# Kernel tuning notes

Hardware: AMD Instinct MI355X
Metric: run time of the kernel (lower is better)

Reference implementation:

```python
import jax, jax.numpy as jnp
import numpy as np

SAMPLE_RATE = 256
WIN = 64          # round(256*250/1000)
HOP = 32          # round(256*125/1000)
HIDDEN = 512
PER_CHAN = 8
MAX_CH = 64
_EEG_BANDS = ((0.5, 4.0), (4.0, 8.0), (8.0, 13.0), (13.0, 30.0), (30.0, 100.0))

_FREQS = np.fft.rfftfreq(WIN, d=1.0 / SAMPLE_RATE)
_BAND_MASKS = [np.logical_and(_FREQS >= lo, _FREQS < hi) for (lo, hi) in _EEG_BANDS]


def _sinusoidal_1d(n, dim, dtype=jnp.float32):
    pos = jnp.arange(n, dtype=jnp.float32)[:, None]
    half = dim // 2
    div = jnp.exp(jnp.arange(half, dtype=jnp.float32) * (-np.log(10000.0) / half))
    ang = pos * div[None, :]
    pe = jnp.zeros((n, dim), dtype=jnp.float32)
    pe = pe.at[:, 0::2].set(jnp.sin(ang))
    pe = pe.at[:, 1::2].set(jnp.cos(ang))
    return pe.astype(dtype)


def setup_inputs() -> dict:
    key = jax.random.key(0)
    k = jax.random.split(key, 5)
    B, T, C = 8, 65536, 64
    return {
        "signal": jax.random.normal(k[0], (B, T, C), dtype=jnp.float32),
        "chan_w": 0.02 * jax.random.normal(k[1], (MAX_CH, 7, PER_CHAN), dtype=jnp.float32),
        "chan_b": 0.02 * jax.random.normal(k[2], (MAX_CH, PER_CHAN), dtype=jnp.float32),
        "mix_w": 0.02 * jax.random.normal(k[3], (HIDDEN, MAX_CH * PER_CHAN), dtype=jnp.float32),
        "marker": 0.02 * jax.random.normal(k[4], (HIDDEN,), dtype=jnp.float32),
    }


def reference(signal, chan_w, chan_b, mix_w, marker):
    B, T, C = signal.shape  # C == MAX_CH, no padding/mask branch
    Tw = (T - WIN) // HOP + 1
    idx = jnp.arange(Tw)[:, None] * HOP + jnp.arange(WIN)[None, :]
    x = jnp.transpose(signal[:, idx, :], (0, 1, 3, 2))
    # spectral features
    mag = jnp.abs(jnp.fft.rfft(x, axis=-1))
    band_feats = jnp.stack(
        [mag[..., m].mean(axis=-1) if m.any() else jnp.zeros(mag.shape[:-1], mag.dtype)
         for m in _BAND_MASKS],
        axis=-1,
    )  # (B, Tw, C, 5)
    mean = x.mean(axis=-1, keepdims=True)
    std = jnp.std(x, axis=-1, ddof=1, keepdims=True)  # torch std is unbiased
    feats = jnp.concatenate([band_feats, mean, std], axis=-1)  # (B, Tw, C, 7)
    # per-channel projection + bias
    emb = jnp.einsum("btcf,cfp->btcp", feats, chan_w) + chan_b[None, None]
    flat = emb.reshape(B, Tw, MAX_CH * PER_CHAN)
    z = flat @ mix_w.T  # (B, Tw, HIDDEN)
    z = z + _sinusoidal_1d(Tw, HIDDEN, z.dtype)[None]
    mk = jnp.broadcast_to(marker[None, None, :], (B, 1, HIDDEN))
    return jnp.concatenate([mk, z], axis=1)  # (B, 1+Tw, HIDDEN)
```

## Files before the change

### kernel.cpp

```cpp
#include <hip/hip_runtime.h>
#include <hip/hip_bf16.h>
#include <stdint.h>

#define TW_N 2047
#define BATCH 8
#define T_LEN 65536
#define NCH 64
#define HID 512
#define NWIN (BATCH * TW_N)

typedef unsigned short ushortT;

__device__ __forceinline__ ushortT f2b(float f) {
  union { float f; uint32_t i; } v; v.f = f;
  uint32_t r = v.i + 0x7fffu + ((v.i >> 16) & 1u);
  return (ushortT)(r >> 16);
}
__device__ __forceinline__ uint32_t pk2(float lo, float hi) {
  return (uint32_t)f2b(lo) | ((uint32_t)f2b(hi) << 16);
}

constexpr float CQ[17] = {
  1.0f, 0.9951847267f, 0.9807852804f, 0.9569403357f, 0.9238795325f,
  0.8819212643f, 0.8314696123f, 0.7730104534f, 0.7071067812f, 0.6343932842f,
  0.5555702330f, 0.4713967368f, 0.3826834324f, 0.2902846773f, 0.1950903220f,
  0.0980171403f, 0.0f };
constexpr float cos64(int m) {
  m &= 63;
  return (m <= 16) ? CQ[m] : (m < 32) ? -CQ[32 - m] : (m < 48) ? -CQ[m - 32] : CQ[64 - m];
}
constexpr float sin64(int m) { return cos64(m - 16); }
struct TwTab { float c[24][32]; float s[24][32]; };
constexpr TwTab make_tab() {
  TwTab t{};
  for (int i = 0; i < 24; ++i)
    for (int j = 0; j < 32; ++j) {
      int m = ((i + 1) * j) & 63;
      t.c[i][j] = cos64(m);
      t.s[i][j] = sin64(m);
    }
  return t;
}
constexpr TwTab TT = make_tab();

__global__ __launch_bounds__(256) void marker_kernel(
    const float* __restrict__ marker, float* __restrict__ out)
{
  const int idx = blockIdx.x * 256 + threadIdx.x;
  out[(size_t)(idx >> 9) * (2048 * 512) + (idx & 511)] = marker[idx & 511];
}

__global__ __launch_bounds__(256) void feat_embed_kernel(
    const float* __restrict__ sig, const float* __restrict__ chw,
    const float* __restrict__ chb, ushortT* __restrict__ flatB)
{
  const int wv = threadIdx.x >> 6;
  const int c = threadIdx.x & 63;
  const int w = blockIdx.x * 4 + wv;
  const int b = w / TW_N;
  const int tw = w - b * TW_N;
  const size_t base = ((size_t)(b * T_LEN + tw * 32)) * NCH + c;

  float x[64];
#pragma unroll
  for (int t = 0; t < 64; ++t) x[t] = sig[base + (size_t)t * NCH];

  float sum = 0.f, sumsq = 0.f;
#pragma unroll
  for (int t = 0; t < 64; ++t) { sum += x[t]; sumsq = fmaf(x[t], x[t], sumsq); }

  float e[32], o[32];
#pragma unroll
  for (int t = 0; t < 32; ++t) { e[t] = x[t] + x[t + 32]; o[t] = x[t] - x[t + 32]; }

  float b1 = 0.f, b2 = 0.f, b3 = 0.f, b4 = 0.f;
#pragma unroll
  for (int i = 0; i < 24; ++i) {
    const int k = i + 1;
    float re = 0.f, im = 0.f;
#pragma unroll
    for (int t = 0; t < 32; ++t) {
      const float v = (k & 1) ? o[t] : e[t];
      re = fmaf(v, TT.c[i][t], re);
      im = fmaf(v, TT.s[i][t], im);
    }
    const float mag = sqrtf(fmaf(re, re, im * im));
    if (k == 1) b1 += mag;
    else if (k < 4) b2 += mag;
    else if (k < 8) b3 += mag;
    else b4 += mag;
  }

  const float mean = sum * (1.f / 64.f);
  const float var = (sumsq - sum * sum * (1.f / 64.f)) * (1.f / 63.f);
  const float sd = sqrtf(fmaxf(var, 0.f));

  float feats[7];
  feats[0] = 0.f;
  feats[1] = b1;
  feats[2] = b2 * 0.5f;
  feats[3] = b3 * 0.25f;
  feats[4] = b4 * (1.f / 17.f);
  feats[5] = mean;
  feats[6] = sd;

  const float* wr = chw + c * 56;
  float emb[8];
#pragma unroll
  for (int p = 0; p < 8; ++p) emb[p] = chb[c * 8 + p];
#pragma unroll
  for (int f = 1; f < 7; ++f) {
    const float fv = feats[f];
#pragma unroll
    for (int p = 0; p < 8; ++p) emb[p] = fmaf(fv, wr[f * 8 + p], emb[p]);
  }

  uint32_t pka[4];
#pragma unroll
  for (int q = 0; q < 4; ++q) pka[q] = pk2(emb[2 * q], emb[2 * q + 1]);
  *(uint4*)(flatB + (size_t)w * HID + c * 8) = make_uint4(pka[0], pka[1], pka[2], pka[3]);
}

typedef __attribute__((ext_vector_type(8))) short short8;
typedef __attribute__((ext_vector_type(4))) float f32x4;

__global__ __launch_bounds__(256) void mix_gemm_kernel(
    const ushortT* __restrict__ A,
    const float* __restrict__ Bw,
    float* __restrict__ out)
{
  __shared__ ushortT As[128 * 32];
  __shared__ ushortT Bs[128 * 32];

  const int tid = threadIdx.x;
  const int lane = tid & 63;
  const int wv = tid >> 6;
  const int wm = wv >> 1, wn = wv & 1;
  const int fr = lane & 15;
  const int fq = lane >> 4;

  const int n0 = blockIdx.x * 128;
  const int m0 = blockIdx.y * 128;

  const int srow = tid >> 2;
  const int sko = (tid & 3) << 3;

  f32x4 acc[4][4];
#pragma unroll
  for (int i = 0; i < 4; ++i)
#pragma unroll
    for (int j = 0; j < 4; ++j) acc[i][j] = (f32x4){0.f, 0.f, 0.f, 0.f};

  uint4 ra[2];
  float4 rbf[2][2];
#pragma unroll
  for (int p = 0; p < 2; ++p) {
    int am = m0 + p * 64 + srow; am = am < (NWIN - 1) ? am : (NWIN - 1);
    ra[p] = *(const uint4*)(A + (size_t)am * HID + sko);
    const float* src = Bw + (size_t)(n0 + p * 64 + srow) * HID + sko;
    rbf[p][0] = *(const float4*)src;
    rbf[p][1] = *(const float4*)(src + 4);
  }

  for (int kt = 0; kt < 16; ++kt) {
#pragma unroll
    for (int p = 0; p < 2; ++p) {
      *(uint4*)&As[(p * 64 + srow) * 32 + sko] = ra[p];
      uint4 bb;
      bb.x = pk2(rbf[p][0].x, rbf[p][0].y);
      bb.y = pk2(rbf[p][0].z, rbf[p][0].w);
      bb.z = pk2(rbf[p][1].x, rbf[p][1].y);
      bb.w = pk2(rbf[p][1].z, rbf[p][1].w);
      *(uint4*)&Bs[(p * 64 + srow) * 32 + sko] = bb;
    }
    __syncthreads();
    if (kt < 15) {
      const int k0 = (kt + 1) * 32;
#pragma unroll
      for (int p = 0; p < 2; ++p) {
        int am = m0 + p * 64 + srow; am = am < (NWIN - 1) ? am : (NWIN - 1);
        ra[p] = *(const uint4*)(A + (size_t)am * HID + k0 + sko);
        const float* src = Bw + (size_t)(n0 + p * 64 + srow) * HID + k0 + sko;
        rbf[p][0] = *(const float4*)src;
        rbf[p][1] = *(const float4*)(src + 4);
      }
    }
    short8 af[4], bf[4];
#pragma unroll
    for (int mt = 0; mt < 4; ++mt)
      af[mt] = *(const short8*)&As[(wm * 64 + mt * 16 + fr) * 32 + fq * 8];
#pragma unroll
    for (int nt = 0; nt < 4; ++nt)
      bf[nt] = *(const short8*)&Bs[(wn * 64 + nt * 16 + fr) * 32 + fq * 8];
#pragma unroll
    for (int mt = 0; mt < 4; ++mt)
#pragma unroll
      for (int nt = 0; nt < 4; ++nt)
        acc[mt][nt] = __builtin_amdgcn_mfma_f32_16x16x32_bf16(af[mt], bf[nt], acc[mt][nt], 0, 0, 0);
    __syncthreads();
  }

#pragma unroll
  for (int nt = 0; nt < 4; ++nt) {
    const int ng = n0 + wn * 64 + nt * 16 + fr;
    const float dv = __expf(-0.03597789208f * (float)(ng >> 1));
    const bool odd = (ng & 1);
#pragma unroll
    for (int mt = 0; mt < 4; ++mt) {
#pragma unroll
      for (int r = 0; r < 4; ++r) {
        const int mg = m0 + wm * 64 + mt * 16 + fq * 4 + r;
        if (mg < NWIN) {
          const int bb = mg / TW_N;
          const int tw = mg - bb * TW_N;
          const float ang = (float)tw * dv;
          const float pev = odd ? __cosf(ang) : __sinf(ang);
          out[((size_t)(bb * 2048 + 1 + tw)) * HID + ng] = acc[mt][nt][r] + pev;
        }
      }
    }
  }
}

extern "C" void kernel_launch(void* const* d_in, const int* in_sizes, int n_in,
                              void* d_out, int out_size, void* d_ws, size_t ws_size,
                              hipStream_t stream)
{
  const float* sig = (const float*)d_in[0];
  const float* chw = (const float*)d_in[1];
  const float* chb = (const float*)d_in[2];
  const float* mxw = (const float*)d_in[3];
  const float* mkr = (const float*)d_in[4];
  float* out = (float*)d_out;

  ushortT* flatB = (ushortT*)d_ws;

  hipLaunchKernelGGL(marker_kernel, dim3(16), dim3(256), 0, stream, mkr, out);
  hipLaunchKernelGGL(feat_embed_kernel, dim3(4094), dim3(256), 0, stream, sig, chw, chb, flatB);
  hipLaunchKernelGGL(mix_gemm_kernel, dim3(4, 128), dim3(256), 0, stream, flatB, mxw, out);
}
```

Measured before the change: 262.1 us.

## Stage signal tiles via LDS, prepack weights to bf16, double-buffer GEMM with direct loads

The feature kernel now loads a shared tile of the signal into LDS with global_load_lds, so the overlapping windows (50% overlap) of 8 windows per block are fetched once instead of twice. A prep kernel converts mix_w to bf16 once per call and also writes the marker rows. The GEMM then streams bf16 A and B tiles straight into double-buffered LDS with async direct loads and manual waitcnt/barriers, removing the per-tile fp32 conversion and register staging. The cost is an extra global buffer and hand-written synchronisation that relies on the vmcnt counts being right.

Result: no change. 266.2 us (+1.5%).

```diff
diff --git a/kernel.cpp b/kernel.cpp
--- a/kernel.cpp
+++ b/kernel.cpp
@@ -1,5 +1,4 @@
 #include <hip/hip_runtime.h>
-#include <hip/hip_bf16.h>
 #include <stdint.h>
 
 #define TW_N 2047
@@ -18,6 +17,12 @@
 }
 __device__ __forceinline__ uint32_t pk2(float lo, float hi) {
   return (uint32_t)f2b(lo) | ((uint32_t)f2b(hi) << 16);
+}
+
+__device__ __forceinline__ void gload_lds16(const void* g, void* l) {
+  __builtin_amdgcn_global_load_lds(
+      (const __attribute__((address_space(1))) uint32_t*)g,
+      (__attribute__((address_space(3))) uint32_t*)l, 16, 0, 0);
 }
 
 constexpr float CQ[17] = {
@@ -43,35 +48,66 @@
 }
 constexpr TwTab TT = make_tab();
 
-__global__ __launch_bounds__(256) void marker_kernel(
-    const float* __restrict__ marker, float* __restrict__ out)
-{
-  const int idx = blockIdx.x * 256 + threadIdx.x;
-  out[(size_t)(idx >> 9) * (2048 * 512) + (idx & 511)] = marker[idx & 511];
-}
-
-__global__ __launch_bounds__(256) void feat_embed_kernel(
+__device__ ushortT Bpack[HID * HID];
+
+__global__ __launch_bounds__(256) void prep_kernel(
+    const float* __restrict__ marker, const float* __restrict__ Bw,
+    float* __restrict__ out)
+{
+  const int gid = blockIdx.x * 256 + threadIdx.x;
+  if (blockIdx.x < 16) {
+    out[(size_t)(gid >> 9) * (2048 * 512) + (gid & 511)] = marker[gid & 511];
+  } else {
+    const int i = (gid - 4096) * 8;
+    const float4 f0 = *(const float4*)(Bw + i);
+    const float4 f1 = *(const float4*)(Bw + i + 4);
+    uint4 u;
+    u.x = pk2(f0.x, f0.y); u.y = pk2(f0.z, f0.w);
+    u.z = pk2(f1.x, f1.y); u.w = pk2(f1.z, f1.w);
+    *(uint4*)(Bpack + i) = u;
+  }
+}
+
+#define WPB 8
+#define SROWS 288
+
+__global__ __launch_bounds__(512) void feat_embed_kernel(
     const float* __restrict__ sig, const float* __restrict__ chw,
     const float* __restrict__ chb, ushortT* __restrict__ flatB)
 {
-  const int wv = threadIdx.x >> 6;
-  const int c = threadIdx.x & 63;
-  const int w = blockIdx.x * 4 + wv;
-  const int b = w / TW_N;
-  const int tw = w - b * TW_N;
-  const size_t base = ((size_t)(b * T_LEN + tw * 32)) * NCH + c;
-
-  float x[64];
-#pragma unroll
-  for (int t = 0; t < 64; ++t) x[t] = sig[base + (size_t)t * NCH];
-
+  __shared__ float xs[SROWS * NCH];
+  const int tid = threadIdx.x;
+  const int tile = blockIdx.x;
+  const int b = blockIdx.y;
+  const int t0 = tile * (WPB * 32);
+
+  const float* sgb = sig + (size_t)b * T_LEN * NCH;
+#pragma unroll
+  for (int k = 0; k < 9; ++k) {
+    const int idx = tid + k * 512;
+    int row = t0 + (idx >> 4);
+    row = row < T_LEN ? row : T_LEN - 1;
+    gload_lds16(sgb + (size_t)row * NCH + (idx & 15) * 4, (char*)xs + (size_t)idx * 16);
+  }
+  __syncthreads();
+
+  const int wv = tid >> 6;
+  const int c = tid & 63;
+  int wl = tile * WPB + wv;
+  wl = wl < TW_N ? wl : TW_N - 1;
+  const int lv = wl - tile * WPB;
+  const float* base = xs + lv * (32 * NCH) + c;
+
+  float e[32], o[32];
   float sum = 0.f, sumsq = 0.f;
 #pragma unroll
-  for (int t = 0; t < 64; ++t) { sum += x[t]; sumsq = fmaf(x[t], x[t], sumsq); }
-
-  float e[32], o[32];
-#pragma unroll
-  for (int t = 0; t < 32; ++t) { e[t] = x[t] + x[t + 32]; o[t] = x[t] - x[t + 32]; }
+  for (int t = 0; t < 32; ++t) {
+    const float a = base[t * 64];
+    const float d = base[(t + 32) * 64];
+    e[t] = a + d; o[t] = a - d;
+    sum += e[t];
+    sumsq = fmaf(a, a, fmaf(d, d, sumsq));
+  }
 
   float b1 = 0.f, b2 = 0.f, b3 = 0.f, b4 = 0.f;
 #pragma unroll
@@ -118,6 +154,7 @@
   uint32_t pka[4];
 #pragma unroll
   for (int q = 0; q < 4; ++q) pka[q] = pk2(emb[2 * q], emb[2 * q + 1]);
+  const int w = b * TW_N + wl;
   *(uint4*)(flatB + (size_t)w * HID + c * 8) = make_uint4(pka[0], pka[1], pka[2], pka[3]);
 }
 
@@ -126,11 +163,10 @@
 
 __global__ __launch_bounds__(256) void mix_gemm_kernel(
     const ushortT* __restrict__ A,
-    const float* __restrict__ Bw,
     float* __restrict__ out)
 {
-  __shared__ ushortT As[128 * 32];
-  __shared__ ushortT Bs[128 * 32];
+  __shared__ ushortT As[2][128 * 32];
+  __shared__ ushortT Bs[2][128 * 32];
 
   const int tid = threadIdx.x;
   const int lane = tid & 63;
@@ -143,7 +179,7 @@
   const int m0 = blockIdx.y * 128;
 
   const int srow = tid >> 2;
-  const int sko = (tid & 3) << 3;
+  const int sko = (tid & 3) * 8;
 
   f32x4 acc[4][4];
 #pragma unroll
@@ -151,54 +187,48 @@
 #pragma unroll
     for (int j = 0; j < 4; ++j) acc[i][j] = (f32x4){0.f, 0.f, 0.f, 0.f};
 
-  uint4 ra[2];
-  float4 rbf[2][2];
-#pragma unroll
-  for (int p = 0; p < 2; ++p) {
-    int am = m0 + p * 64 + srow; am = am < (NWIN - 1) ? am : (NWIN - 1);
-    ra[p] = *(const uint4*)(A + (size_t)am * HID + sko);
-    const float* src = Bw + (size_t)(n0 + p * 64 + srow) * HID + sko;
-    rbf[p][0] = *(const float4*)src;
-    rbf[p][1] = *(const float4*)(src + 4);
-  }
+  int am0 = m0 + srow;       am0 = am0 < NWIN ? am0 : NWIN - 1;
+  int am1 = m0 + 64 + srow;  am1 = am1 < NWIN ? am1 : NWIN - 1;
+  const ushortT* ga0 = A + (size_t)am0 * HID + sko;
+  const ushortT* ga1 = A + (size_t)am1 * HID + sko;
+  const ushortT* gb0 = Bpack + (size_t)(n0 + srow) * HID + sko;
+  const ushortT* gb1 = Bpack + (size_t)(n0 + 64 + srow) * HID + sko;
+
+#define STAGE(buf, kt) do {                                                    \
+    const int ko_ = (kt) * 32;                                                 \
+    gload_lds16(ga0 + ko_, (char*)&As[buf][0] + tid * 16);                     \
+    gload_lds16(ga1 + ko_, (char*)&As[buf][0] + 4096 + tid * 16);              \
+    gload_lds16(gb0 + ko_, (char*)&Bs[buf][0] + tid * 16);                     \
+    gload_lds16(gb1 + ko_, (char*)&Bs[buf][0] + 4096 + tid * 16);              \
+  } while (0)
+
+  STAGE(0, 0);
 
   for (int kt = 0; kt < 16; ++kt) {
-#pragma unroll
-    for (int p = 0; p < 2; ++p) {
-      *(uint4*)&As[(p * 64 + srow) * 32 + sko] = ra[p];
-      uint4 bb;
-      bb.x = pk2(rbf[p][0].x, rbf[p][0].y);
-      bb.y = pk2(rbf[p][0].z, rbf[p][0].w);
-      bb.z = pk2(rbf[p][1].x, rbf[p][1].y);
-      bb.w = pk2(rbf[p][1].z, rbf[p][1].w);
-      *(uint4*)&Bs[(p * 64 + srow) * 32 + sko] = bb;
-    }
-    __syncthreads();
+    const int cur = kt & 1;
     if (kt < 15) {
-      const int k0 = (kt + 1) * 32;
-#pragma unroll
-      for (int p = 0; p < 2; ++p) {
-        int am = m0 + p * 64 + srow; am = am < (NWIN - 1) ? am : (NWIN - 1);
-        ra[p] = *(const uint4*)(A + (size_t)am * HID + k0 + sko);
-        const float* src = Bw + (size_t)(n0 + p * 64 + srow) * HID + k0 + sko;
-        rbf[p][0] = *(const float4*)src;
-        rbf[p][1] = *(const float4*)(src + 4);
-      }
-    }
+      STAGE(cur ^ 1, kt + 1);
+      asm volatile("s_waitcnt vmcnt(4)\n\ts_barrier" ::: "memory");
+    } else {
+      asm volatile("s_waitcnt vmcnt(0)\n\ts_barrier" ::: "memory");
+    }
+
     short8 af[4], bf[4];
 #pragma unroll
     for (int mt = 0; mt < 4; ++mt)
-      af[mt] = *(const short8*)&As[(wm * 64 + mt * 16 + fr) * 32 + fq * 8];
+      af[mt] = *(const short8*)&As[cur][(wm * 64 + mt * 16 + fr) * 32 + fq * 8];
 #pragma unroll
     for (int nt = 0; nt < 4; ++nt)
-      bf[nt] = *(const short8*)&Bs[(wn * 64 + nt * 16 + fr) * 32 + fq * 8];
+      bf[nt] = *(const short8*)&Bs[cur][(wn * 64 + nt * 16 + fr) * 32 + fq * 8];
 #pragma unroll
     for (int mt = 0; mt < 4; ++mt)
 #pragma unroll
       for (int nt = 0; nt < 4; ++nt)
         acc[mt][nt] = __builtin_amdgcn_mfma_f32_16x16x32_bf16(af[mt], bf[nt], acc[mt][nt], 0, 0, 0);
-    __syncthreads();
-  }
+
+    asm volatile("s_barrier" ::: "memory");
+  }
+#undef STAGE
 
 #pragma unroll
   for (int nt = 0; nt < 4; ++nt) {
@@ -235,7 +265,7 @@
 
   ushortT* flatB = (ushortT*)d_ws;
 
-  hipLaunchKernelGGL(marker_kernel, dim3(16), dim3(256), 0, stream, mkr, out);
-  hipLaunchKernelGGL(feat_embed_kernel, dim3(4094), dim3(256), 0, stream, sig, chw, chb, flatB);
-  hipLaunchKernelGGL(mix_gemm_kernel, dim3(4, 128), dim3(256), 0, stream, flatB, mxw, out);
-}
+  hipLaunchKernelGGL(prep_kernel, dim3(144), dim3(256), 0, stream, mkr, mxw, out);
+  hipLaunchKernelGGL(feat_embed_kernel, dim3(256, 8), dim3(512), 0, stream, sig, chw, chb, flatB);
+  hipLaunchKernelGGL(mix_gemm_kernel, dim3(4, 128), dim3(256), 0, stream, flatB, out);
+}
```
